# Optimization experiments

Hardware: AMD Instinct MI355X
Metric: run time of the kernel (lower is better)

The kernel has to match this reference:

```python
import jax, jax.numpy as jnp
import numpy as np
import math

B, N, IN_DIM = 128, 100, 8
E, H, FF, L = 512, 8, 2048, 6
DH = E // H
MAX_STEPS = int(N * 1.5)
EPS = 1e-5

def _ln(x, g, b):
    mu = x.mean(-1, keepdims=True)
    var = ((x - mu) ** 2).mean(-1, keepdims=True)
    return (x - mu) / jnp.sqrt(var + EPS) * g + b

def _mha(q_in, k_in, v_in, wq, bq, wk, bk, wv, bv, wo, bo):
    Bq, Sq = q_in.shape[0], q_in.shape[1]
    q = (q_in @ wq + bq).reshape(Bq, Sq, H, DH)
    k = (k_in @ wk + bk).reshape(Bq, -1, H, DH)
    v = (v_in @ wv + bv).reshape(Bq, -1, H, DH)
    s = jnp.einsum('bqhd,bkhd->bhqk', q, k) / math.sqrt(DH)
    a = jax.nn.softmax(s, axis=-1)
    o = jnp.einsum('bhqk,bkhd->bqhd', a, v).reshape(Bq, Sq, E)
    return o @ wo + bo

def setup_inputs():
    key = jax.random.key(0)
    keys = iter(jax.random.split(key, 64))
    def nrm(shape, s=0.02):
        return jax.random.normal(next(keys), shape, jnp.float32) * s
    d = {}
    d['node_features'] = jax.random.normal(next(keys), (B, N, IN_DIM), jnp.float32)
    d['edge_weights'] = jax.random.uniform(next(keys), (B, N, N), jnp.float32)
    pos = np.arange(N)[:, None].astype(np.float32)
    div = np.exp(np.arange(0, E, 2).astype(np.float32) * (-math.log(10000.0) / E))
    pe = np.zeros((N, E), np.float32)
    pe[:, 0::2] = np.sin(pos * div); pe[:, 1::2] = np.cos(pos * div)
    d['pe'] = jnp.asarray(pe)
    d['in_w'] = nrm((IN_DIM, E)); d['in_b'] = jnp.zeros((E,), jnp.float32)
    for nm in ['enc_wq', 'enc_wk', 'enc_wv', 'enc_wo']:
        d[nm] = nrm((L, E, E))
    for nm in ['enc_bq', 'enc_bk', 'enc_bv', 'enc_bo']:
        d[nm] = jnp.zeros((L, E), jnp.float32)
    d['enc_w1'] = nrm((L, E, FF)); d['enc_b1'] = jnp.zeros((L, FF), jnp.float32)
    d['enc_w2'] = nrm((L, FF, E)); d['enc_b2'] = jnp.zeros((L, E), jnp.float32)
    d['enc_ln1g'] = jnp.ones((L, E), jnp.float32); d['enc_ln1b'] = jnp.zeros((L, E), jnp.float32)
    d['enc_ln2g'] = jnp.ones((L, E), jnp.float32); d['enc_ln2b'] = jnp.zeros((L, E), jnp.float32)
    d['lstm_wih'] = nrm((E, 4 * E)); d['lstm_whh'] = nrm((E, 4 * E))
    d['lstm_bih'] = jnp.zeros((4 * E,), jnp.float32); d['lstm_bhh'] = jnp.zeros((4 * E,), jnp.float32)
    for nm in ['dec_wq', 'dec_wk', 'dec_wv', 'dec_wo', 'dec_pw']:
        d[nm] = nrm((E, E))
    for nm in ['dec_bq', 'dec_bk', 'dec_bv', 'dec_bo', 'dec_pb']:
        d[nm] = jnp.zeros((E,), jnp.float32)
    d['dec_lng'] = jnp.ones((E,), jnp.float32); d['dec_lnb'] = jnp.zeros((E,), jnp.float32)
    d['shortcut_bonus'] = jnp.asarray(5.0, jnp.float32)
    d['revisit_penalty'] = jnp.asarray(-0.5, jnp.float32)
    d['done_w'] = nrm((E, 1)); d['done_b'] = jnp.zeros((1,), jnp.float32)
    return d

def _forward(node_features, edge_weights, pe, in_w, in_b, enc_wq, enc_bq, enc_wk, enc_bk, enc_wv, enc_bv, enc_wo, enc_bo, enc_w1, enc_b1, enc_w2, enc_b2, enc_ln1g, enc_ln1b, enc_ln2g, enc_ln2b, lstm_wih, lstm_whh, lstm_bih, lstm_bhh, dec_wq, dec_bq, dec_wk, dec_bk, dec_wv, dec_bv, dec_wo, dec_bo, dec_pw, dec_pb, dec_lng, dec_lnb, shortcut_bonus, revisit_penalty, done_w, done_b):
    # ---- Encoder (dropout = eval-mode identity) ----
    x = node_features @ in_w + in_b + pe[:N]
    for l in range(L):
        attn = _mha(x, x, x, enc_wq[l], enc_bq[l], enc_wk[l], enc_bk[l], enc_wv[l], enc_bv[l], enc_wo[l], enc_bo[l])
        x = _ln(x + attn, enc_ln1g[l], enc_ln1b[l])
        ff = jax.nn.relu(x @ enc_w1[l] + enc_b1[l]) @ enc_w2[l] + enc_b2[l]
        x = _ln(x + ff, enc_ln2g[l], enc_ln2b[l])
    node_emb = x  # [B, N, E]

    ar = jnp.arange(N)
    ew_to_first = edge_weights[:, :, 0]  # dist(mid -> node 0), [B, N]

    def step_fn(carry, step):
        h, c, ctx, visited, ucount, complete, all_vis, first, prev = carry
        # LSTMCell, torch gate order (i, f, g, o)
        gates = ctx @ lstm_wih + lstm_bih + h @ lstm_whh + lstm_bhh
        i_g, f_g, g_g, o_g = jnp.split(gates, 4, axis=-1)
        c2 = jax.nn.sigmoid(f_g) * c + jax.nn.sigmoid(i_g) * jnp.tanh(g_g)
        h2 = jax.nn.sigmoid(o_g) * jnp.tanh(c2)
        # greedy done-predictor: stop if sigmoid(logit) > 0.5 once tour can be closed
        done_p = jax.nn.sigmoid(h2 @ done_w + done_b)[:, 0]
        eligible = (~complete) & (ucount >= N) & (step >= N)
        complete = complete | (eligible & (done_p > 0.5))
        # DecoderStep: 1-query attention over node embeddings
        a = _mha(h2[:, None, :], node_emb, node_emb, dec_wq, dec_bq, dec_wk, dec_bk, dec_wv, dec_bv, dec_wo, dec_bo)[:, 0]
        a = _ln(a, dec_lng, dec_lnb)
        logits = a @ dec_pw + dec_pb
        scores = jnp.einsum('be,bne->bn', logits, node_emb)
        # revisit penalty while tour incomplete (vectorized masked_fill_)
        scores = jnp.where((~all_vis)[:, None] & visited, revisit_penalty, scores)
        # shortcut bonus once all nodes visited (vectorized gather over edge_weights)
        ew_prev = jnp.take_along_axis(edge_weights, prev[:, None, None], axis=1)[:, 0, :]  # [B, N] row dist(prev -> *)
        direct = ew_prev[:, :1]                      # dist(prev -> 0)
        via = ew_prev + ew_to_first                  # dist(prev -> mid) + dist(mid -> 0)
        bonus = jnp.where(via < direct, shortcut_bonus * (direct - via) / direct, 0.0)
        scores = scores + jnp.where(all_vis[:, None], bonus, 0.0)
        # completed tours: force return to first node
        scores = jnp.where(complete[:, None], -1e9, scores)
        scores = jnp.where(complete[:, None] & (ar[None, :] == first[:, None]), 100.0, scores)
        probs = jax.nn.softmax(scores, axis=1)
        curr = jnp.argmax(probs, axis=1).astype(jnp.int32)  # greedy selection
        logp = jnp.log(jnp.take_along_axis(probs, curr[:, None], 1)[:, 0] + 1e-10)
        first = jnp.where(step == 0, curr, first)
        # state updates (guarded by active, as in the torch per-batch loop)
        active = ~complete
        cur_mask = ar[None, :] == curr[:, None]
        newly = active & ~jnp.take_along_axis(visited, curr[:, None], 1)[:, 0]
        ucount = ucount + newly.astype(jnp.int32)
        visited = visited | (active[:, None] & cur_mask)
        all_vis = all_vis | (ucount >= N)
        ctx2 = jnp.take_along_axis(node_emb, curr[:, None, None], axis=1)[:, 0, :]
        return (h2, c2, ctx2, visited, ucount, complete, all_vis, first, curr), (curr, logp)

    carry0 = (jnp.zeros((B, E), jnp.float32), jnp.zeros((B, E), jnp.float32), node_emb.mean(1),
              jnp.zeros((B, N), bool), jnp.zeros((B,), jnp.int32),
              jnp.zeros((B,), bool), jnp.zeros((B,), bool),
              jnp.zeros((B,), jnp.int32), jnp.zeros((B,), jnp.int32))
    carry, (tours, logps) = jax.lax.scan(step_fn, carry0, jnp.arange(MAX_STEPS))
    complete, first = carry[5], carry[7]
    # final forced step (step == max_steps in torch): incomplete tours return to first node, logp = 0
    final_node = jnp.where(complete, jnp.int32(0), first)
    tours = jnp.concatenate([tours, final_node[None]], 0)                 # [MAX_STEPS+1, B]
    logps = jnp.concatenate([logps, jnp.zeros((1, B), jnp.float32)], 0)   # [MAX_STEPS+1, B]
    return logps, tours

def reference(node_features, edge_weights, pe, in_w, in_b, enc_wq, enc_bq, enc_wk, enc_bk, enc_wv, enc_bv, enc_wo, enc_bo, enc_w1, enc_b1, enc_w2, enc_b2, enc_ln1g, enc_ln1b, enc_ln2g, enc_ln2b, lstm_wih, lstm_whh, lstm_bih, lstm_bhh, dec_wq, dec_bq, dec_wk, dec_bk, dec_wv, dec_bv, dec_wo, dec_bo, dec_pw, dec_pb, dec_lng, dec_lnb, shortcut_bonus, revisit_penalty, done_w, done_b):
    return _forward(node_features, edge_weights, pe, in_w, in_b, enc_wq, enc_bq, enc_wk, enc_bk, enc_wv, enc_bv, enc_wo, enc_bo, enc_w1, enc_b1, enc_w2, enc_b2, enc_ln1g, enc_ln1b, enc_ln2g, enc_ln2b, lstm_wih, lstm_whh, lstm_bih, lstm_bhh, dec_wq, dec_bq, dec_wk, dec_bk, dec_wv, dec_bv, dec_wo, dec_bo, dec_pw, dec_pb, dec_lng, dec_lnb, shortcut_bonus, revisit_penalty, done_w, done_b)
```

## Files before the change

kernel.cpp:

```cpp
#include <hip/hip_runtime.h>
#include <math.h>

#define Bb 128
#define Nn 100
#define Ee 512
#define Hh 8
#define DHd 64
#define FFf 2048
#define Ll 6
#define STEPS 150

typedef _Float16 h8 __attribute__((ext_vector_type(8)));
typedef _Float16 h4 __attribute__((ext_vector_type(4)));
typedef float f4 __attribute__((ext_vector_type(4)));

template<bool RELU, bool BIAS, bool OUTF32, bool SPLITK>
__global__ __launch_bounds__(256) void mgemm_k(
    const _Float16* __restrict__ Ah, const _Float16* __restrict__ Al, int lda,
    const _Float16* __restrict__ Bh, const _Float16* __restrict__ Bl, int ldb,
    float* __restrict__ C, _Float16* __restrict__ Ch, _Float16* __restrict__ Cl,
    int ldc, const float* __restrict__ bias, int K, int kc, int Mtot)
{
  __shared__ _Float16 sm[4 * 5120];
  _Float16* sAh = sm;
// ... 169 lines not shown
  for (int idx = t; idx < 6400; idx += 256) {
    int i = idx >> 6, d = idx & 63;
    qs[i * 68 + d]  = qg[(size_t)i * 512 + d];
    kT[d * 113 + i] = kg[(size_t)i * 512 + d];
  }
  __syncthreads();
  int ti = t >> 4, tj = t & 15;
  int i0 = ti * 7, j0 = tj * 7;
  float s[7][7];
#pragma unroll
  for (int r = 0; r < 7; ++r)
#pragma unroll
    for (int c = 0; c < 7; ++c) s[r][c] = 0.f;
  for (int kk = 0; kk < 64; ++kk) {
    float a[7], bb[7];
#pragma unroll
    for (int r = 0; r < 7; ++r) a[r] = qs[(i0 + r) * 68 + kk];
#pragma unroll
    for (int c = 0; c < 7; ++c) bb[c] = kT[kk * 113 + j0 + c];
#pragma unroll
    for (int r = 0; r < 7; ++r)
#pragma unroll
      for (int c = 0; c < 7; ++c) s[r][c] += a[r] * bb[c];
  }
  __syncthreads();
#pragma unroll
  for (int r = 0; r < 7; ++r)
#pragma unroll
    for (int c = 0; c < 7; ++c) {
      int i = i0 + r, j = j0 + c;
      if (i < Nn && j < Nn) p[i * 104 + j] = s[r][c] * 0.125f;
    }
  __syncthreads();
  int w = t >> 6, lane = t & 63;
  for (int i = w; i < Nn; i += 4) {
    float x0 = p[i * 104 + lane];
    float x1 = (lane < 36) ? p[i * 104 + 64 + lane] : -3.4e38f;
    float mx = fmaxf(x0, x1);
    for (int msk = 32; msk; msk >>= 1) mx = fmaxf(mx, __shfl_xor(mx, msk));
    float e0 = expf(x0 - mx);
    float e1 = (lane < 36) ? expf(x1 - mx) : 0.f;
    float ss = e0 + e1;
    for (int msk = 32; msk; msk >>= 1) ss += __shfl_xor(ss, msk);
    p[i * 104 + lane] = e0 / ss;
    if (lane < 36) p[i * 104 + 64 + lane] = e1 / ss;
  }
  __syncthreads();
  int d0 = tj * 4;
  float oa[7][4];
#pragma unroll
  for (int r = 0; r < 7; ++r)
#pragma unroll
    for (int c = 0; c < 4; ++c) oa[r][c] = 0.f;
  for (int j = 0; j < Nn; ++j) {
    float pr[7];
#pragma unroll
    for (int r = 0; r < 7; ++r) pr[r] = p[(i0 + r) * 104 + j];
    float4 vv = *(const float4*)(vg + (size_t)j * 512 + d0);
#pragma unroll
    for (int r = 0; r < 7; ++r) {
      oa[r][0] += pr[r] * vv.x; oa[r][1] += pr[r] * vv.y;
      oa[r][2] += pr[r] * vv.z; oa[r][3] += pr[r] * vv.w;
    }
  }
  size_t ob = ((size_t)b * Nn) * 512 + h * 64 + d0;
#pragma unroll
  for (int r = 0; r < 7; ++r)
    if (i0 + r < Nn) {
      h4 hv, lv;
#pragma unroll
      for (int c = 0; c < 4; ++c) {
        _Float16 hh = (_Float16)oa[r][c];
        hv[c] = hh;
        lv[c] = (_Float16)(oa[r][c] - (float)hh);
      }
      *(h4*)(oh + ob + (size_t)(i0 + r) * 512) = hv;
      *(h4*)(ol + ob + (size_t)(i0 + r) * 512) = lv;
    }
}

template<int BM, int BN, int BK, int TM, int TN>
__global__ __launch_bounds__(256) void gemm_k(
    const float* __restrict__ A, int lda,
    const float* __restrict__ B1, const float* __restrict__ B2, int splitB, int ldb,
    float* __restrict__ C, int ldc, int M, int N, int K, int kChunk)
{
  __shared__ __align__(16) float As[BK][BM + 4];
  __shared__ __align__(16) float Bs[BK][BN + 4];
  const int tid = threadIdx.x;
  const int m0 = blockIdx.y * BM;
  const int n0 = blockIdx.x * BN;
  const int k0 = blockIdx.z * kChunk;
  const int kEnd = k0 + kChunk;
  constexpr int TCOLS = BN / TN;
  const int tm = tid / TCOLS;
  const int tn = tid % TCOLS;
  float acc[TM][TN];
#pragma unroll
  for (int i = 0; i < TM; ++i)
#pragma unroll
    for (int j = 0; j < TN; ++j) acc[i][j] = 0.f;

  for (int kt = k0; kt < kEnd; kt += BK) {
    constexpr int A4 = BM * BK / 4;
    for (int c = tid; c < A4; c += 256) {
      int mm = c / (BK / 4);
      int k4 = (c % (BK / 4)) * 4;
      float4 av = *(const float4*)(A + (size_t)(m0 + mm) * lda + kt + k4);
      As[k4 + 0][mm] = av.x;
      As[k4 + 1][mm] = av.y;
      As[k4 + 2][mm] = av.z;
      As[k4 + 3][mm] = av.w;
    }
    constexpr int B4 = BK * BN / 4;
    for (int c = tid; c < B4; c += 256) {
      int kk = c / (BN / 4);
      int n4 = (c % (BN / 4)) * 4;
      int kgi = kt + kk;
      const float* Brow = (kgi < splitB) ? (B1 + (size_t)kgi * ldb)
                                         : (B2 + (size_t)(kgi - splitB) * ldb);
      *(float4*)&Bs[kk][n4] = *(const float4*)(Brow + n0 + n4);
    }
    __syncthreads();
#pragma unroll
    for (int kk = 0; kk < BK; ++kk) {
      float a[TM], b[TN];
#pragma unroll
      for (int i = 0; i < TM; ++i) a[i] = As[kk][tm * TM + i];
#pragma unroll
      for (int j = 0; j < TN; ++j) b[j] = Bs[kk][tn * TN + j];
#pragma unroll
      for (int i = 0; i < TM; ++i)
#pragma unroll
        for (int j = 0; j < TN; ++j)
          acc[i][j] += a[i] * b[j];
    }
    __syncthreads();
  }

  float* Cout = C + (size_t)blockIdx.z * (size_t)M * ldc;
#pragma unroll
  for (int i = 0; i < TM; ++i) {
    int m = m0 + tm * TM + i;
#pragma unroll
    for (int j = 0; j < TN; j += 4) {
      int n = n0 + tn * TN + j;
      float4 r;
      r.x = acc[i][j + 0]; r.y = acc[i][j + 1]; r.z = acc[i][j + 2]; r.w = acc[i][j + 3];
      *(float4*)(Cout + (size_t)m * ldc + n) = r;
    }
  }
}

__global__ __launch_bounds__(256) void init_k(
    const float* __restrict__ emb, float* __restrict__ ctxh, float* __restrict__ cbuf,
    int* visited, int* ucount, int* complete, int* allvis, int* first, int* prev,
    float* out)
{
  int b = blockIdx.x, t = threadIdx.x;
#pragma unroll
  for (int r = 0; r < 2; ++r) {
    int e = t + 256 * r;
    float s = 0.f;
    for (int i = 0; i < Nn; ++i) s += emb[((size_t)b * Nn + i) * 512 + e];
    ctxh[(size_t)b * 1024 + e] = s / 100.f;
    ctxh[(size_t)b * 1024 + 512 + e] = 0.f;
    cbuf[(size_t)b * 512 + e] = 0.f;
  }
  if (t < Nn) visited[b * Nn + t] = 0;
  if (t == 0) {
    ucount[b] = 0; complete[b] = 0; allvis[b] = 0; first[b] = 0; prev[b] = 0;
    out[150 * Bb + b] = 0.f;
  }
}

__device__ __forceinline__ float sigm(float x) { return 1.f / (1.f + expf(-x)); }

__global__ __launch_bounds__(256) void lstm_pw_k(
    const float* __restrict__ gP, const float* __restrict__ bih, const float* __restrict__ bhh,
    float* __restrict__ ctxh, float* __restrict__ cbuf,
    const float* __restrict__ done_w, const float* __restrict__ done_b,
    int* complete, const int* ucount, int step)
{
  int b = blockIdx.x, t = threadIdx.x;
  __shared__ float red[256];
  const float* g0 = gP + (size_t)b * 2048;
  const float* g1 = gP + 262144 + (size_t)b * 2048;
  float dsum = 0.f;
#pragma unroll
  for (int r = 0; r < 2; ++r) {
    int e = t + 256 * r;
    float ig = g0[e] + g1[e] + bih[e] + bhh[e];
    float fg = g0[e + 512] + g1[e + 512] + bih[e + 512] + bhh[e + 512];
    float gg = g0[e + 1024] + g1[e + 1024] + bih[e + 1024] + bhh[e + 1024];
    float og = g0[e + 1536] + g1[e + 1536] + bih[e + 1536] + bhh[e + 1536];
    float cprev = cbuf[(size_t)b * 512 + e];
    float c2 = sigm(fg) * cprev + sigm(ig) * tanhf(gg);
    float h2 = sigm(og) * tanhf(c2);
    cbuf[(size_t)b * 512 + e] = c2;
    ctxh[(size_t)b * 1024 + 512 + e] = h2;
    dsum += h2 * done_w[e];
  }
  red[t] = dsum; __syncthreads();
  for (int o = 128; o > 0; o >>= 1) { if (t < o) red[t] += red[t + o]; __syncthreads(); }
  if (t == 0) {
    float z = red[0] + done_b[0];
    if (!complete[b] && ucount[b] >= Nn && step >= Nn && z > 0.f) complete[b] = 1;
  }
}

__global__ __launch_bounds__(128) void dec_attn_k(
    const float* __restrict__ qP, const float* __restrict__ bq,
    const float* __restrict__ Kd, const float* __restrict__ Vd,
    float* __restrict__ o)
{
  int bh = blockIdx.x; int b = bh >> 3, h = bh & 7;
  int t = threadIdx.x;
  __shared__ float qh[64];
  __shared__ float p[100];
  __shared__ float red[128];
  if (t < 64) {
    float s = bq[h * 64 + t];
#pragma unroll
    for (int s8 = 0; s8 < 8; ++s8) s += qP[(size_t)s8 * 65536 + (size_t)b * 512 + h * 64 + t];
    qh[t] = s;
  }
  __syncthreads();
  float scv = -3.4e38f;
  if (t < Nn) {
    const float* kr = Kd + ((size_t)b * Nn + t) * 512 + h * 64;
    float s = 0.f;
#pragma unroll
    for (int d = 0; d < 64; ++d) s += qh[d] * kr[d];
    scv = s * 0.125f;
  }
  red[t] = scv; __syncthreads();
  for (int o2 = 64; o2 > 0; o2 >>= 1) { if (t < o2) red[t] = fmaxf(red[t], red[t + o2]); __syncthreads(); }
  float m = red[0]; __syncthreads();
  float ex = (t < Nn) ? expf(scv - m) : 0.f;
  red[t] = ex; __syncthreads();
  for (int o2 = 64; o2 > 0; o2 >>= 1) { if (t < o2) red[t] += red[t + o2]; __syncthreads(); }
  float Z = red[0];
  if (t < Nn) p[t] = ex / Z;
  __syncthreads();
  if (t < 64) {
    float acc = 0.f;
    const float* vr = Vd + (size_t)b * Nn * 512 + h * 64 + t;
    for (int j = 0; j < Nn; ++j) acc += p[j] * vr[(size_t)j * 512];
    o[(size_t)b * 512 + h * 64 + t] = acc;
  }
}

__global__ __launch_bounds__(256) void dec_ln_k(
    const float* __restrict__ woP, const float* __restrict__ bo,
    const float* __restrict__ g, const float* __restrict__ bb,
    float* __restrict__ out)
{
  int b = blockIdx.x, t = threadIdx.x;
  __shared__ float red[256];
  float v[2];
#pragma unroll
  for (int r = 0; r < 2; ++r) {
    int e = t + 256 * r;
    float s = bo[e];
#pragma unroll
    for (int s8 = 0; s8 < 8; ++s8) s += woP[(size_t)s8 * 65536 + (size_t)b * 512 + e];
    v[r] = s;
  }
  red[t] = v[0] + v[1]; __syncthreads();
  for (int o = 128; o > 0; o >>= 1) { if (t < o) red[t] += red[t + o]; __syncthreads(); }
  float mu = red[0] * (1.f / 512.f);
  __syncthreads();
  float d0 = v[0] - mu, d1 = v[1] - mu;
  red[t] = d0 * d0 + d1 * d1; __syncthreads();
  for (int o = 128; o > 0; o >>= 1) { if (t < o) red[t] += red[t + o]; __syncthreads(); }
  float inv = 1.f / sqrtf(red[0] * (1.f / 512.f) + 1e-5f);
  out[(size_t)b * 512 + t] = d0 * inv * g[t] + bb[t];
  out[(size_t)b * 512 + t + 256] = d1 * inv * g[t + 256] + bb[t + 256];
}

__global__ __launch_bounds__(256) void select_k(
    const float* __restrict__ pwP, const float* __restrict__ pb,
    const float* __restrict__ emb, const float* __restrict__ ew,
    int* visited, int* ucount, int* complete, int* allvis, int* first, int* prev,
    float* __restrict__ ctxh, float* __restrict__ out,
    const float* __restrict__ sb_p, const float* __restrict__ rp_p, int step)
{
  int b = blockIdx.x, t = threadIdx.x;
  __shared__ float logits[512];
  __shared__ float sc[128];
  __shared__ float red[256];
  __shared__ int redi[256];
#pragma unroll
  for (int r = 0; r < 2; ++r) {
    int e = t + 256 * r;
    float s = pb[e];
#pragma unroll
    for (int s8 = 0; s8 < 8; ++s8) s += pwP[(size_t)s8 * 65536 + (size_t)b * 512 + e];
    logits[e] = s;
  }
  __syncthreads();
  if (t < Nn) {
    const float* er = emb + ((size_t)b * Nn + t) * 512;
    float s = 0.f;
    for (int e = 0; e < 512; ++e) s += logits[e] * er[e];
    int av = allvis[b];
    if (!av && visited[b * Nn + t]) s = rp_p[0];
    if (av) {
      int pv = prev[b];
      float direct = ew[(size_t)b * 10000 + (size_t)pv * 100];
      float via = ew[(size_t)b * 10000 + (size_t)pv * 100 + t] + ew[(size_t)b * 10000 + (size_t)t * 100];
      if (via < direct) s += sb_p[0] * (direct - via) / direct;
    }
    if (complete[b]) s = (t == first[b]) ? 100.f : -1e9f;
    sc[t] = s;
  }
  __syncthreads();
  float vv = (t < Nn) ? sc[t] : -3.4e38f;
  int ii = (t < Nn) ? t : 0x7fffffff;
  red[t] = vv; redi[t] = ii;
  __syncthreads();
  for (int o = 128; o > 0; o >>= 1) {
    if (t < o) {
      float v2 = red[t + o]; int i2 = redi[t + o];
      if (v2 > red[t] || (v2 == red[t] && i2 < redi[t])) { red[t] = v2; redi[t] = i2; }
    }
    __syncthreads();
  }
  float m = red[0];
  int curr = redi[0];
  __syncthreads();
  float ex = (t < Nn) ? expf(sc[t] - m) : 0.f;
  red[t] = ex; __syncthreads();
  for (int o = 128; o > 0; o >>= 1) { if (t < o) red[t] += red[t + o]; __syncthreads(); }
  float Z = red[0];
  if (t == 0) {
    float pcur = expf(sc[curr] - m) / Z;
    out[step * Bb + b] = logf(pcur + 1e-10f);
    out[(151 + step) * Bb + b] = (float)curr;
    if (!complete[b]) {
      if (!visited[b * Nn + curr]) ucount[b] = ucount[b] + 1;
      visited[b * Nn + curr] = 1;
    }
    if (ucount[b] >= Nn) allvis[b] = 1;
    if (step == 0) first[b] = curr;
    prev[b] = curr;
  }
  const float* src = emb + ((size_t)b * Nn + curr) * 512;
  ctxh[(size_t)b * 1024 + t] = src[t];
  ctxh[(size_t)b * 1024 + t + 256] = src[t + 256];
}

__global__ void final_k(const int* complete, const int* first, float* out)
{
  int b = threadIdx.x;
  out[(151 + 150) * Bb + b] = complete[b] ? 0.f : (float)first[b];
}

extern "C" void kernel_launch(void* const* d_in, const int* in_sizes, int n_in,
                              void* d_out, int out_size, void* d_ws, size_t ws_size,
                              hipStream_t stream)
{
  const float* nf      = (const float*)d_in[0];
  const float* ew      = (const float*)d_in[1];
  const float* pe      = (const float*)d_in[2];
  const float* in_w    = (const float*)d_in[3];
  const float* in_b    = (const float*)d_in[4];
  const float* enc_wq  = (const float*)d_in[5];
  const float* enc_wk  = (const float*)d_in[6];
  const float* enc_wv  = (const float*)d_in[7];
  const float* enc_wo  = (const float*)d_in[8];
  const float* enc_bq  = (const float*)d_in[9];
  const float* enc_bk  = (const float*)d_in[10];
  const float* enc_bv  = (const float*)d_in[11];
  const float* enc_bo  = (const float*)d_in[12];
  const float* enc_w1  = (const float*)d_in[13];
  const float* enc_b1  = (const float*)d_in[14];
  const float* enc_w2  = (const float*)d_in[15];
  const float* enc_b2  = (const float*)d_in[16];
  const float* ln1g    = (const float*)d_in[17];
  const float* ln1b    = (const float*)d_in[18];
  const float* ln2g    = (const float*)d_in[19];
  const float* ln2b    = (const float*)d_in[20];
  const float* wih     = (const float*)d_in[21];
  const float* whh     = (const float*)d_in[22];
  const float* bih     = (const float*)d_in[23];
  const float* bhh     = (const float*)d_in[24];
  const float* dwq     = (const float*)d_in[25];
  const float* dwk     = (const float*)d_in[26];
  const float* dwv     = (const float*)d_in[27];
  const float* dwo     = (const float*)d_in[28];
  const float* dpw     = (const float*)d_in[29];
  const float* dbq     = (const float*)d_in[30];
  const float* dbk     = (const float*)d_in[31];
  const float* dbv     = (const float*)d_in[32];
  const float* dbo     = (const float*)d_in[33];
  const float* dpb     = (const float*)d_in[34];
  const float* dlng    = (const float*)d_in[35];
  const float* dlnb    = (const float*)d_in[36];
  const float* sbp     = (const float*)d_in[37];
  const float* rpp     = (const float*)d_in[38];
  const float* done_w  = (const float*)d_in[39];
  const float* done_b  = (const float*)d_in[40];
  float* out = (float*)d_out;

  const size_t SZ = 12800ull * 512;
  float* ws = (float*)d_ws;
  float* x   = ws;
  float* xq  = x + SZ;
  float* xk  = xq + SZ;
  float* xv  = xk + SZ;
  _Float16* xh = (_Float16*)(xv + SZ);
  _Float16* xl = xh + SZ;
  _Float16* oh = xl + SZ;
  _Float16* ol = oh + SZ;
  _Float16* wb = ol + SZ;
  _Float16* wqh = wb;               _Float16* wql = wqh + 262144;
  _Float16* wkh = wql + 262144;     _Float16* wkl = wkh + 262144;
  _Float16* wvh = wkl + 262144;     _Float16* wvl = wvh + 262144;
  _Float16* woh_ = wvl + 262144;    _Float16* wol_ = woh_ + 262144;
  _Float16* w1h = wol_ + 262144;    _Float16* w1l = w1h + 1048576;
  _Float16* w2h = w1l + 1048576;    _Float16* w2l = w2h + 1048576;
  float* ctxh   = (float*)(w2l + 1048576);
  float* cbuf   = ctxh + 131072;
  float* gatesP = cbuf + 65536;
  float* qP     = gatesP + 524288;
  float* woP    = qP + 524288;
  float* pwP    = woP + 524288;
  float* abuf   = pwP + 524288;
  float* dbuf   = abuf + 65536;
  int* ivis     = (int*)(dbuf + 65536);
  int* ucount   = ivis + 12800;
  int* complete = ucount + 128;
  int* allvis   = complete + 128;
  int* first    = allvis + 128;
  int* prev     = first + 128;

  input_proj_k<<<25600, 256, 0, stream>>>(nf, in_w, in_b, pe, x, xh, xl);

  for (int l = 0; l < Ll; ++l) {
    const float* wq = enc_wq + (size_t)l * 262144;
    const float* wk = enc_wk + (size_t)l * 262144;
    const float* wv = enc_wv + (size_t)l * 262144;
    const float* wo = enc_wo + (size_t)l * 262144;
    const float* bq = enc_bq + (size_t)l * 512;
    const float* bk = enc_bk + (size_t)l * 512;
    const float* bv = enc_bv + (size_t)l * 512;
    const float* bo = enc_bo + (size_t)l * 512;
    const float* w1 = enc_w1 + (size_t)l * 1048576;
    const float* b1 = enc_b1 + (size_t)l * 2048;
    const float* w2 = enc_w2 + (size_t)l * 1048576;
    const float* b2 = enc_b2 + (size_t)l * 512;

    wconv_k<<<dim3(16, 16), 256, 0, stream>>>(wq, 512, 512, wqh, wql);
    wconv_k<<<dim3(16, 16), 256, 0, stream>>>(wk, 512, 512, wkh, wkl);
    wconv_k<<<dim3(16, 16), 256, 0, stream>>>(wv, 512, 512, wvh, wvl);
    wconv_k<<<dim3(16, 16), 256, 0, stream>>>(wo, 512, 512, woh_, wol_);
    wconv_k<<<dim3(64, 16), 256, 0, stream>>>(w1, 512, 2048, w1h, w1l);
    wconv_k<<<dim3(16, 64), 256, 0, stream>>>(w2, 2048, 512, w2h, w2l);

    mgemm_k<false, true, true, false><<<dim3(4, 100), 256, 0, stream>>>(
        xh, xl, 512, wqh, wql, 512, xq, nullptr, nullptr, 512, bq, 512, 0, 0);
    mgemm_k<false, true, true, false><<<dim3(4, 100), 256, 0, stream>>>(
        xh, xl, 512, wkh, wkl, 512, xk, nullptr, nullptr, 512, bk, 512, 0, 0);
    mgemm_k<false, true, true, false><<<dim3(4, 100), 256, 0, stream>>>(
        xh, xl, 512, wvh, wvl, 512, xv, nullptr, nullptr, 512, bv, 512, 0, 0);
    enc_attn_k<<<1024, 256, 0, stream>>>(xq, xk, xv, oh, ol);
    mgemm_k<false, true, true, false><<<dim3(4, 100), 256, 0, stream>>>(
        oh, ol, 512, woh_, wol_, 512, xq, nullptr, nullptr, 512, bo, 512, 0, 0);
    ln_k<<<12800, 256, 0, stream>>>(x, xq, ln1g + l * 512, ln1b + l * 512, x, xh, xl);
    for (int c = 0; c < 4; ++c) {
      mgemm_k<true, true, false, false><<<dim3(16, 25), 256, 0, stream>>>(
          xh + (size_t)c * 3200 * 512, xl + (size_t)c * 3200 * 512, 512,
          w1h, w1l, 512, nullptr, oh, ol, 2048, b1, 512, 0, 0);
      mgemm_k<false, false, true, true><<<dim3(4, 25, 4), 256, 0, stream>>>(
          oh, ol, 2048, w2h, w2l, 2048, xv, nullptr, nullptr, 512,
          nullptr, 2048, 512, 3200);
      reduce4_k<<<6400, 256, 0, stream>>>(xv, b2, xq + (size_t)c * 3200 * 512);
    }
    ln_k<<<12800, 256, 0, stream>>>(x, xq, ln2g + l * 512, ln2b + l * 512, x, xh, xl);
  }

  wconv_k<<<dim3(16, 16), 256, 0, stream>>>(dwk, 512, 512, wqh, wql);
  wconv_k<<<dim3(16, 16), 256, 0, stream>>>(dwv, 512, 512, wkh, wkl);
  mgemm_k<false, true, true, false><<<dim3(4, 100), 256, 0, stream>>>(
      xh, xl, 512, wqh, wql, 512, xk, nullptr, nullptr, 512, dbk, 512, 0, 0);
  mgemm_k<false, true, true, false><<<dim3(4, 100), 256, 0, stream>>>(
      xh, xl, 512, wkh, wkl, 512, xv, nullptr, nullptr, 512, dbv, 512, 0, 0);
  init_k<<<128, 256, 0, stream>>>(x, ctxh, cbuf, ivis, ucount, complete, allvis, first, prev, out);

  for (int step = 0; step < STEPS; ++step) {
    gemm_k<32, 64, 16, 2, 4><<<dim3(32, 4, 2), 256, 0, stream>>>(
        ctxh, 1024, wih, whh, 512, 2048, gatesP, 2048, 128, 2048, 1024, 512);
    lstm_pw_k<<<128, 256, 0, stream>>>(gatesP, bih, bhh, ctxh, cbuf, done_w, done_b,
                                       complete, ucount, step);
    gemm_k<32, 64, 16, 2, 4><<<dim3(8, 4, 8), 256, 0, stream>>>(
        ctxh + 512, 1024, dwq, dwq, 1 << 30, 512, qP, 512, 128, 512, 512, 64);
    dec_attn_k<<<1024, 128, 0, stream>>>(qP, dbq, xk, xv, dbuf);
    gemm_k<32, 64, 16, 2, 4><<<dim3(8, 4, 8), 256, 0, stream>>>(
        dbuf, 512, dwo, dwo, 1 << 30, 512, woP, 512, 128, 512, 512, 64);
    dec_ln_k<<<128, 256, 0, stream>>>(woP, dbo, dlng, dlnb, abuf);
    gemm_k<32, 64, 16, 2, 4><<<dim3(8, 4, 8), 256, 0, stream>>>(
        abuf, 512, dpw, dpw, 1 << 30, 512, pwP, 512, 128, 512, 512, 64);
    select_k<<<128, 256, 0, stream>>>(pwP, dpb, x, ew, ivis, ucount, complete, allvis,
                                      first, prev, ctxh, out, sbp, rpp, step);
  }
  final_k<<<1, 128, 0, stream>>>(complete, first, out);
}
```

Baseline: 16.52 ms.

## Fuse LSTM pointwise into query GEMM and fold decoder LayerNorm into projection

The LSTM pointwise update now runs inside the query-projection GEMM, which recomputes h on the fly as its A tile and writes c into a double-buffered cell state. The done-head partial dot products go to a buffer that the select kernel reads to update completion. The decoder LayerNorm is folded algebraically into the pointer projection: the gamma-scaled weight and the gamma/beta correction vectors are precomputed once, and the LN and projection matvec are done inside the select kernel. This cuts three kernel launches and two global round-trips per decode step, at the cost of redundant LSTM math across N-blocks and a serial 512x512 matvec per batch row inside select.

```diff
diff --git a/kernel.cpp b/kernel.cpp
--- a/kernel.cpp
+++ b/kernel.cpp
@@ -345,6 +345,25 @@
   }
 }
 
+__global__ void gscale_k(const float* __restrict__ dpw, const float* __restrict__ g,
+                         float* __restrict__ gpw)
+{
+  int i = blockIdx.x * 256 + threadIdx.x;
+  gpw[i] = g[i >> 9] * dpw[i];
+}
+
+__global__ void uv_k(const float* __restrict__ pw, const float* __restrict__ g,
+                     const float* __restrict__ bb, float* __restrict__ uv)
+{
+  int c = blockIdx.x * 256 + threadIdx.x;
+  float su = 0.f, sw = 0.f;
+  for (int k = 0; k < 512; ++k) {
+    float p = pw[(size_t)k * 512 + c];
+    su += g[k] * p; sw += bb[k] * p;
+  }
+  uv[c] = su; uv[512 + c] = sw;
+}
+
 __global__ __launch_bounds__(256) void init_k(
     const float* __restrict__ emb, float* __restrict__ ctxh, float* __restrict__ cbuf,
     int* visited, int* ucount, int* complete, int* allvis, int* first, int* prev,
@@ -369,36 +388,137 @@
 
 __device__ __forceinline__ float sigm(float x) { return 1.f / (1.f + expf(-x)); }
 
-__global__ __launch_bounds__(256) void lstm_pw_k(
-    const float* __restrict__ gP, const float* __restrict__ bih, const float* __restrict__ bhh,
-    float* __restrict__ ctxh, float* __restrict__ cbuf,
-    const float* __restrict__ done_w, const float* __restrict__ done_b,
-    int* complete, const int* ucount, int step)
-{
-  int b = blockIdx.x, t = threadIdx.x;
-  __shared__ float red[256];
-  const float* g0 = gP + (size_t)b * 2048;
-  const float* g1 = gP + 262144 + (size_t)b * 2048;
-  float dsum = 0.f;
-#pragma unroll
-  for (int r = 0; r < 2; ++r) {
-    int e = t + 256 * r;
-    float ig = g0[e] + g1[e] + bih[e] + bhh[e];
-    float fg = g0[e + 512] + g1[e + 512] + bih[e + 512] + bhh[e + 512];
-    float gg = g0[e + 1024] + g1[e + 1024] + bih[e + 1024] + bhh[e + 1024];
-    float og = g0[e + 1536] + g1[e + 1536] + bih[e + 1536] + bhh[e + 1536];
-    float cprev = cbuf[(size_t)b * 512 + e];
-    float c2 = sigm(fg) * cprev + sigm(ig) * tanhf(gg);
-    float h2 = sigm(og) * tanhf(c2);
-    cbuf[(size_t)b * 512 + e] = c2;
-    ctxh[(size_t)b * 1024 + 512 + e] = h2;
-    dsum += h2 * done_w[e];
-  }
-  red[t] = dsum; __syncthreads();
-  for (int o = 128; o > 0; o >>= 1) { if (t < o) red[t] += red[t + o]; __syncthreads(); }
-  if (t == 0) {
-    float z = red[0] + done_b[0];
-    if (!complete[b] && ucount[b] >= Nn && step >= Nn && z > 0.f) complete[b] = 1;
+__device__ __forceinline__ float4 add44(float4 a, float4 b, float4 c, float4 d)
+{
+  float4 r;
+  r.x = a.x + b.x + c.x + d.x;
+  r.y = a.y + b.y + c.y + d.y;
+  r.z = a.z + b.z + c.z + d.z;
+  r.w = a.w + b.w + c.w + d.w;
+  return r;
+}
+
+__device__ __forceinline__ void lstm4(
+    const float* __restrict__ gP, const float* __restrict__ bih,
+    const float* __restrict__ bhh, const float* __restrict__ cin,
+    int b, int e4, float4* h2o, float4* c2o)
+{
+  const float* g0 = gP + (size_t)b * 2048 + e4;
+  const float* g1 = gP + 262144 + (size_t)b * 2048 + e4;
+  float4 ig = add44(*(const float4*)(g0),
+                    *(const float4*)(g1),
+                    *(const float4*)(bih + e4),
+                    *(const float4*)(bhh + e4));
+  float4 fg = add44(*(const float4*)(g0 + 512),
+                    *(const float4*)(g1 + 512),
+                    *(const float4*)(bih + 512 + e4),
+                    *(const float4*)(bhh + 512 + e4));
+  float4 gg = add44(*(const float4*)(g0 + 1024),
+                    *(const float4*)(g1 + 1024),
+                    *(const float4*)(bih + 1024 + e4),
+                    *(const float4*)(bhh + 1024 + e4));
+  float4 og = add44(*(const float4*)(g0 + 1536),
+                    *(const float4*)(g1 + 1536),
+                    *(const float4*)(bih + 1536 + e4),
+                    *(const float4*)(bhh + 1536 + e4));
+  float4 cp = *(const float4*)(cin + (size_t)b * 512 + e4);
+  float4 c2, h2;
+  c2.x = sigm(fg.x) * cp.x + sigm(ig.x) * tanhf(gg.x);  h2.x = sigm(og.x) * tanhf(c2.x);
+  c2.y = sigm(fg.y) * cp.y + sigm(ig.y) * tanhf(gg.y);  h2.y = sigm(og.y) * tanhf(c2.y);
+  c2.z = sigm(fg.z) * cp.z + sigm(ig.z) * tanhf(gg.z);  h2.z = sigm(og.z) * tanhf(c2.z);
+  c2.w = sigm(fg.w) * cp.w + sigm(ig.w) * tanhf(gg.w);  h2.w = sigm(og.w) * tanhf(c2.w);
+  *h2o = h2; *c2o = c2;
+}
+
+__global__ __launch_bounds__(256) void qh_gemm_k(
+    const float* __restrict__ gP, const float* __restrict__ bih,
+    const float* __restrict__ bhh, const float* __restrict__ cin,
+    float* __restrict__ cout, const float* __restrict__ done_w,
+    float* __restrict__ ctxh, const float* __restrict__ Bw,
+    float* __restrict__ C, float* __restrict__ dpart)
+{
+  __shared__ __align__(16) float As[16][36];
+  __shared__ __align__(16) float Bs[16][68];
+  __shared__ float sPre[32][8];
+  const int tid = threadIdx.x;
+  const int m0 = blockIdx.y * 32;
+  const int n0 = blockIdx.x * 64;
+  const int z  = blockIdx.z;
+  const int k0 = z * 64;
+  const int tm = tid >> 4;
+  const int tn = tid & 15;
+
+  if (blockIdx.x == 0) {
+    int bl = tid >> 3;
+    int el = (tid & 7) * 8;
+    int gb = m0 + bl;
+    float dsum = 0.f;
+#pragma unroll
+    for (int q = 0; q < 2; ++q) {
+      int e = k0 + el + q * 4;
+      float4 h2, c2;
+      lstm4(gP, bih, bhh, cin, gb, e, &h2, &c2);
+      *(float4*)(cout + (size_t)gb * 512 + e) = c2;
+      *(float4*)(ctxh + (size_t)gb * 1024 + 512 + e) = h2;
+      float4 dw = *(const float4*)(done_w + e);
+      dsum += h2.x * dw.x + h2.y * dw.y + h2.z * dw.z + h2.w * dw.w;
+    }
+    sPre[bl][tid & 7] = dsum;
+  }
+  __syncthreads();
+  if (blockIdx.x == 0 && tid < 32) {
+    float s = 0.f;
+#pragma unroll
+    for (int q = 0; q < 8; ++q) s += sPre[tid][q];
+    dpart[z * 128 + m0 + tid] = s;
+  }
+
+  float acc[2][4];
+#pragma unroll
+  for (int i = 0; i < 2; ++i)
+#pragma unroll
+    for (int j = 0; j < 4; ++j) acc[i][j] = 0.f;
+
+  for (int kt = k0; kt < k0 + 64; kt += 16) {
+    if (tid < 128) {
+      int mm = tid >> 2;
+      int k4 = (tid & 3) * 4;
+      float4 h2, c2d;
+      lstm4(gP, bih, bhh, cin, m0 + mm, kt + k4, &h2, &c2d);
+      As[k4 + 0][mm] = h2.x;
+      As[k4 + 1][mm] = h2.y;
+      As[k4 + 2][mm] = h2.z;
+      As[k4 + 3][mm] = h2.w;
+    }
+    {
+      int kk = tid >> 4;
+      int n4 = (tid & 15) * 4;
+      *(float4*)&Bs[kk][n4] = *(const float4*)(Bw + (size_t)(kt + kk) * 512 + n0 + n4);
+    }
+    __syncthreads();
+#pragma unroll
+    for (int kk = 0; kk < 16; ++kk) {
+      float a[2], b[4];
+      a[0] = As[kk][tm * 2 + 0];
+      a[1] = As[kk][tm * 2 + 1];
+#pragma unroll
+      for (int j = 0; j < 4; ++j) b[j] = Bs[kk][tn * 4 + j];
+#pragma unroll
+      for (int i = 0; i < 2; ++i)
+#pragma unroll
+        for (int j = 0; j < 4; ++j) acc[i][j] += a[i] * b[j];
+    }
+    __syncthreads();
+  }
+
+  float* Cout = C + (size_t)z * 128 * 512;
+#pragma unroll
+  for (int i = 0; i < 2; ++i) {
+    int m = m0 + tm * 2 + i;
+    int n = n0 + tn * 4;
+    float4 r;
+    r.x = acc[i][0]; r.y = acc[i][1]; r.z = acc[i][2]; r.w = acc[i][3];
+    *(float4*)(Cout + (size_t)m * 512 + n) = r;
   }
 }
 
@@ -444,59 +564,79 @@
   }
 }
 
-__global__ __launch_bounds__(256) void dec_ln_k(
-    const float* __restrict__ woP, const float* __restrict__ bo,
-    const float* __restrict__ g, const float* __restrict__ bb,
-    float* __restrict__ out)
-{
-  int b = blockIdx.x, t = threadIdx.x;
-  __shared__ float red[256];
-  float v[2];
-#pragma unroll
-  for (int r = 0; r < 2; ++r) {
-    int e = t + 256 * r;
-    float s = bo[e];
-#pragma unroll
-    for (int s8 = 0; s8 < 8; ++s8) s += woP[(size_t)s8 * 65536 + (size_t)b * 512 + e];
-    v[r] = s;
-  }
-  red[t] = v[0] + v[1]; __syncthreads();
-  for (int o = 128; o > 0; o >>= 1) { if (t < o) red[t] += red[t + o]; __syncthreads(); }
-  float mu = red[0] * (1.f / 512.f);
-  __syncthreads();
-  float d0 = v[0] - mu, d1 = v[1] - mu;
-  red[t] = d0 * d0 + d1 * d1; __syncthreads();
-  for (int o = 128; o > 0; o >>= 1) { if (t < o) red[t] += red[t + o]; __syncthreads(); }
-  float inv = 1.f / sqrtf(red[0] * (1.f / 512.f) + 1e-5f);
-  out[(size_t)b * 512 + t] = d0 * inv * g[t] + bb[t];
-  out[(size_t)b * 512 + t + 256] = d1 * inv * g[t + 256] + bb[t + 256];
-}
-
-__global__ __launch_bounds__(256) void select_k(
-    const float* __restrict__ pwP, const float* __restrict__ pb,
+__global__ __launch_bounds__(256) void select3_k(
+    const float* __restrict__ woP, const float* __restrict__ dbo,
+    const float* __restrict__ gpw, const float* __restrict__ uv,
+    const float* __restrict__ dpb,
     const float* __restrict__ emb, const float* __restrict__ ew,
+    const float* __restrict__ dpart, const float* __restrict__ done_b,
     int* visited, int* ucount, int* complete, int* allvis, int* first, int* prev,
     float* __restrict__ ctxh, float* __restrict__ out,
     const float* __restrict__ sb_p, const float* __restrict__ rp_p, int step)
 {
   int b = blockIdx.x, t = threadIdx.x;
-  __shared__ float logits[512];
+  __shared__ __align__(16) float yv[512];
+  __shared__ __align__(16) float lg[512];
   __shared__ float sc[128];
   __shared__ float red[256];
   __shared__ int redi[256];
-#pragma unroll
-  for (int r = 0; r < 2; ++r) {
-    int e = t + 256 * r;
-    float s = pb[e];
-#pragma unroll
-    for (int s8 = 0; s8 < 8; ++s8) s += pwP[(size_t)s8 * 65536 + (size_t)b * 512 + e];
-    logits[e] = s;
-  }
-  __syncthreads();
+  __shared__ int s_cm;
+  __shared__ float s_mu, s_inv;
+
+  if (t == 0) {
+    float dp = 0.f;
+#pragma unroll
+    for (int z = 0; z < 8; ++z) dp += dpart[z * 128 + b];
+    int cm = complete[b];
+    if (!cm && ucount[b] >= Nn && step >= Nn && (dp + done_b[0]) > 0.f) {
+      cm = 1; complete[b] = 1;
+    }
+    s_cm = cm;
+  }
+
+  float v0 = dbo[t], v1 = dbo[t + 256];
+#pragma unroll
+  for (int s8 = 0; s8 < 8; ++s8) {
+    v0 += woP[(size_t)s8 * 65536 + (size_t)b * 512 + t];
+    v1 += woP[(size_t)s8 * 65536 + (size_t)b * 512 + t + 256];
+  }
+  yv[t] = v0; yv[t + 256] = v1;
+  red[t] = v0 + v1; __syncthreads();
+  for (int o = 128; o > 0; o >>= 1) { if (t < o) red[t] += red[t + o]; __syncthreads(); }
+  float mu = red[0] * (1.f / 512.f);
+  __syncthreads();
+  float d0 = v0 - mu, d1 = v1 - mu;
+  red[t] = d0 * d0 + d1 * d1; __syncthreads();
+  for (int o = 128; o > 0; o >>= 1) { if (t < o) red[t] += red[t + o]; __syncthreads(); }
+  if (t == 0) {
+    s_mu = mu;
+    s_inv = 1.f / sqrtf(red[0] * (1.f / 512.f) + 1e-5f);
+  }
+  __syncthreads();
+
+  {
+    float acc0 = 0.f, acc1 = 0.f;
+#pragma unroll 8
+    for (int e = 0; e < 512; ++e) {
+      float ye = yv[e];
+      acc0 += ye * gpw[(size_t)e * 512 + t];
+      acc1 += ye * gpw[(size_t)e * 512 + t + 256];
+    }
+    float inv = s_inv, m2 = s_inv * s_mu;
+    lg[t]       = inv * acc0 - m2 * uv[t]       + uv[512 + t]       + dpb[t];
+    lg[t + 256] = inv * acc1 - m2 * uv[t + 256] + uv[512 + t + 256] + dpb[t + 256];
+  }
+  __syncthreads();
+
   if (t < Nn) {
     const float* er = emb + ((size_t)b * Nn + t) * 512;
     float s = 0.f;
-    for (int e = 0; e < 512; ++e) s += logits[e] * er[e];
+#pragma unroll 8
+    for (int e4 = 0; e4 < 128; ++e4) {
+      float4 ev = *(const float4*)(er + e4 * 4);
+      float4 lv = *(const float4*)(lg + e4 * 4);
+      s += lv.x * ev.x + lv.y * ev.y + lv.z * ev.z + lv.w * ev.w;
+    }
     int av = allvis[b];
     if (!av && visited[b * Nn + t]) s = rp_p[0];
     if (av) {
@@ -505,7 +645,7 @@
       float via = ew[(size_t)b * 10000 + (size_t)pv * 100 + t] + ew[(size_t)b * 10000 + (size_t)t * 100];
       if (via < direct) s += sb_p[0] * (direct - via) / direct;
     }
-    if (complete[b]) s = (t == first[b]) ? 100.f : -1e9f;
+    if (s_cm) s = (t == first[b]) ? 100.f : -1e9f;
     sc[t] = s;
   }
   __syncthreads();
@@ -531,7 +671,7 @@
     float pcur = expf(sc[curr] - m) / Z;
     out[step * Bb + b] = logf(pcur + 1e-10f);
     out[(151 + step) * Bb + b] = (float)curr;
-    if (!complete[b]) {
+    if (!s_cm) {
       if (!visited[b * Nn + curr]) ucount[b] = ucount[b] + 1;
       visited[b * Nn + curr] = 1;
     }
@@ -615,13 +755,15 @@
   _Float16* w1h = wol_ + 262144;    _Float16* w1l = w1h + 1048576;
   _Float16* w2h = w1l + 1048576;    _Float16* w2l = w2h + 1048576;
   float* ctxh   = (float*)(w2l + 1048576);
-  float* cbuf   = ctxh + 131072;
-  float* gatesP = cbuf + 65536;
+  float* cbufA  = ctxh + 131072;
+  float* gatesP = cbufA + 65536;
   float* qP     = gatesP + 524288;
   float* woP    = qP + 524288;
-  float* pwP    = woP + 524288;
-  float* abuf   = pwP + 524288;
-  float* dbuf   = abuf + 65536;
+  float* gpw    = woP + 524288;
+  float* uvv    = gpw + 262144;
+  float* dpart  = uvv + 1024;
+  float* cbufB  = gpw + 524288;
+  float* dbuf   = cbufB + 65536;
   int* ivis     = (int*)(dbuf + 65536);
   int* ucount   = ivis + 12800;
   int* complete = ucount + 128;
@@ -680,23 +822,24 @@
       xh, xl, 512, wqh, wql, 512, xk, nullptr, nullptr, 512, dbk, 512, 0, 0);
   mgemm_k<false, true, true, false><<<dim3(4, 100), 256, 0, stream>>>(
       xh, xl, 512, wkh, wkl, 512, xv, nullptr, nullptr, 512, dbv, 512, 0, 0);
-  init_k<<<128, 256, 0, stream>>>(x, ctxh, cbuf, ivis, ucount, complete, allvis, first, prev, out);
-
+  gscale_k<<<1024, 256, 0, stream>>>(dpw, dlng, gpw);
+  uv_k<<<2, 256, 0, stream>>>(dpw, dlng, dlnb, uvv);
+  init_k<<<128, 256, 0, stream>>>(x, ctxh, cbufA, ivis, ucount, complete, allvis, first, prev, out);
+
+  float* cin = cbufA;
+  float* cout = cbufB;
   for (int step = 0; step < STEPS; ++step) {
     gemm_k<32, 64, 16, 2, 4><<<dim3(32, 4, 2), 256, 0, stream>>>(
         ctxh, 1024, wih, whh, 512, 2048, gatesP, 2048, 128, 2048, 1024, 512);
-    lstm_pw_k<<<128, 256, 0, stream>>>(gatesP, bih, bhh, ctxh, cbuf, done_w, done_b,
-                                       complete, ucount, step);
-    gemm_k<32, 64, 16, 2, 4><<<dim3(8, 4, 8), 256, 0, stream>>>(
-        ctxh + 512, 1024, dwq, dwq, 1 << 30, 512, qP, 512, 128, 512, 512, 64);
+    qh_gemm_k<<<dim3(8, 4, 8), 256, 0, stream>>>(
+        gatesP, bih, bhh, cin, cout, done_w, ctxh, dwq, qP, dpart);
     dec_attn_k<<<1024, 128, 0, stream>>>(qP, dbq, xk, xv, dbuf);
     gemm_k<32, 64, 16, 2, 4><<<dim3(8, 4, 8), 256, 0, stream>>>(
         dbuf, 512, dwo, dwo, 1 << 30, 512, woP, 512, 128, 512, 512, 64);
-    dec_ln_k<<<128, 256, 0, stream>>>(woP, dbo, dlng, dlnb, abuf);
-    gemm_k<32, 64, 16, 2, 4><<<dim3(8, 4, 8), 256, 0, stream>>>(
-        abuf, 512, dpw, dpw, 1 << 30, 512, pwP, 512, 128, 512, 512, 64);
-    select_k<<<128, 256, 0, stream>>>(pwP, dpb, x, ew, ivis, ucount, complete, allvis,
-                                      first, prev, ctxh, out, sbp, rpp, step);
+    select3_k<<<128, 256, 0, stream>>>(woP, dbo, gpw, uvv, dpb, x, ew, dpart, done_b,
+                                       ivis, ucount, complete, allvis, first, prev,
+                                       ctxh, out, sbp, rpp, step);
+    float* tmp = cin; cin = cout; cout = tmp;
   }
   final_k<<<1, 128, 0, stream>>>(complete, first, out);
 }
```

New measurement: 20.04 ms. +21.3%, slower.

## Fuse LSTM gate GEMM with pointwise cell update using interleaved gate weights

Applied to the files above, without the earlier changes.

Builds an interleaved weight matrix so each output column group holds the i/f/g/o gates of one hidden unit. The LSTM gate GEMM and pointwise cell update then run in a single kernel per step, replacing a split-K GEMM plus a separate pointwise kernel and removing the gatesP round trip. The hidden state is double-buffered across steps to avoid a read/write race. The done-probe reduction moves into select_k via per-block partial sums. The fused kernel loses split-K parallelism (128 blocks over K=1024), which may lengthen the per-step serial chain.

```diff
diff --git a/kernel.cpp b/kernel.cpp
--- a/kernel.cpp
+++ b/kernel.cpp
@@ -345,6 +345,17 @@
   }
 }
 
+__global__ void wg2build_k(const float* __restrict__ wih, const float* __restrict__ whh,
+                           float* __restrict__ Wg2)
+{
+  int idx = blockIdx.x * 256 + threadIdx.x;
+  int k = idx >> 9, e = idx & 511;
+  const float* src = (k < 512) ? (wih + (size_t)k * 2048) : (whh + (size_t)(k - 512) * 2048);
+  float4 o;
+  o.x = src[e]; o.y = src[512 + e]; o.z = src[1024 + e]; o.w = src[1536 + e];
+  *(float4*)(Wg2 + (size_t)k * 2048 + e * 4) = o;
+}
+
 __global__ __launch_bounds__(256) void init_k(
     const float* __restrict__ emb, float* __restrict__ ctxh, float* __restrict__ cbuf,
     int* visited, int* ucount, int* complete, int* allvis, int* first, int* prev,
@@ -356,8 +367,8 @@
     int e = t + 256 * r;
     float s = 0.f;
     for (int i = 0; i < Nn; ++i) s += emb[((size_t)b * Nn + i) * 512 + e];
-    ctxh[(size_t)b * 1024 + e] = s / 100.f;
-    ctxh[(size_t)b * 1024 + 512 + e] = 0.f;
+    ctxh[(size_t)b * 1536 + e] = s / 100.f;
+    ctxh[(size_t)b * 1536 + 512 + e] = 0.f;
     cbuf[(size_t)b * 512 + e] = 0.f;
   }
   if (t < Nn) visited[b * Nn + t] = 0;
@@ -369,36 +380,85 @@
 
 __device__ __forceinline__ float sigm(float x) { return 1.f / (1.f + expf(-x)); }
 
-__global__ __launch_bounds__(256) void lstm_pw_k(
-    const float* __restrict__ gP, const float* __restrict__ bih, const float* __restrict__ bhh,
-    float* __restrict__ ctxh, float* __restrict__ cbuf,
-    const float* __restrict__ done_w, const float* __restrict__ done_b,
-    int* complete, const int* ucount, int step)
-{
-  int b = blockIdx.x, t = threadIdx.x;
-  __shared__ float red[256];
-  const float* g0 = gP + (size_t)b * 2048;
-  const float* g1 = gP + 262144 + (size_t)b * 2048;
-  float dsum = 0.f;
-#pragma unroll
-  for (int r = 0; r < 2; ++r) {
-    int e = t + 256 * r;
-    float ig = g0[e] + g1[e] + bih[e] + bhh[e];
-    float fg = g0[e + 512] + g1[e + 512] + bih[e + 512] + bhh[e + 512];
-    float gg = g0[e + 1024] + g1[e + 1024] + bih[e + 1024] + bhh[e + 1024];
-    float og = g0[e + 1536] + g1[e + 1536] + bih[e + 1536] + bhh[e + 1536];
-    float cprev = cbuf[(size_t)b * 512 + e];
-    float c2 = sigm(fg) * cprev + sigm(ig) * tanhf(gg);
+__global__ __launch_bounds__(256) void gateslstm_k(
+    const float* __restrict__ ctxh_c, const float* __restrict__ Wg2,
+    const float* __restrict__ bih, const float* __restrict__ bhh,
+    float* __restrict__ cbuf, const float* __restrict__ done_w,
+    float* __restrict__ ctxh_w, float* __restrict__ dpart, int hin)
+{
+  __shared__ __align__(16) float As[16][36];
+  __shared__ __align__(16) float Bs[16][68];
+  __shared__ float sDD[32][17];
+  const int tid = threadIdx.x;
+  const int m0 = blockIdx.y * 32;
+  const int n0 = blockIdx.x * 64;
+  const int tm = tid >> 4;
+  const int tn = tid & 15;
+  float acc[2][4];
+#pragma unroll
+  for (int i = 0; i < 2; ++i)
+#pragma unroll
+    for (int j = 0; j < 4; ++j) acc[i][j] = 0.f;
+
+  for (int kt = 0; kt < 1024; kt += 16) {
+    const int akt = kt + ((kt >= 512) ? 512 * hin : 0);
+    if (tid < 128) {
+      int mm = tid >> 2;
+      int k4 = (tid & 3) * 4;
+      float4 av = *(const float4*)(ctxh_c + (size_t)(m0 + mm) * 1536 + akt + k4);
+      As[k4 + 0][mm] = av.x;
+      As[k4 + 1][mm] = av.y;
+      As[k4 + 2][mm] = av.z;
+      As[k4 + 3][mm] = av.w;
+    }
+    {
+      int kk = tid >> 4;
+      int n4 = (tid & 15) * 4;
+      *(float4*)&Bs[kk][n4] = *(const float4*)(Wg2 + (size_t)(kt + kk) * 2048 + n0 + n4);
+    }
+    __syncthreads();
+#pragma unroll
+    for (int kk = 0; kk < 16; ++kk) {
+      float a[2], b[4];
+      a[0] = As[kk][tm * 2 + 0];
+      a[1] = As[kk][tm * 2 + 1];
+#pragma unroll
+      for (int j = 0; j < 4; ++j) b[j] = Bs[kk][tn * 4 + j];
+#pragma unroll
+      for (int i = 0; i < 2; ++i)
+#pragma unroll
+        for (int j = 0; j < 4; ++j) acc[i][j] += a[i] * b[j];
+    }
+    __syncthreads();
+  }
+
+  const int e = (n0 >> 2) + tn;
+  const float bi0 = bih[e],        bh0 = bhh[e];
+  const float bi1 = bih[512 + e],  bh1 = bhh[512 + e];
+  const float bi2 = bih[1024 + e], bh2 = bhh[1024 + e];
+  const float bi3 = bih[1536 + e], bh3 = bhh[1536 + e];
+  const float dw = done_w[e];
+  const int hwoff = 512 + 512 * (hin ^ 1);
+#pragma unroll
+  for (int i = 0; i < 2; ++i) {
+    int b = m0 + tm * 2 + i;
+    float ig = acc[i][0] + bi0 + bh0;
+    float fg = acc[i][1] + bi1 + bh1;
+    float gg = acc[i][2] + bi2 + bh2;
+    float og = acc[i][3] + bi3 + bh3;
+    float cp = cbuf[(size_t)b * 512 + e];
+    float c2 = sigm(fg) * cp + sigm(ig) * tanhf(gg);
     float h2 = sigm(og) * tanhf(c2);
     cbuf[(size_t)b * 512 + e] = c2;
-    ctxh[(size_t)b * 1024 + 512 + e] = h2;
-    dsum += h2 * done_w[e];
-  }
-  red[t] = dsum; __syncthreads();
-  for (int o = 128; o > 0; o >>= 1) { if (t < o) red[t] += red[t + o]; __syncthreads(); }
-  if (t == 0) {
-    float z = red[0] + done_b[0];
-    if (!complete[b] && ucount[b] >= Nn && step >= Nn && z > 0.f) complete[b] = 1;
+    ctxh_w[(size_t)b * 1536 + hwoff + e] = h2;
+    sDD[tm * 2 + i][tn] = h2 * dw;
+  }
+  __syncthreads();
+  if (tid < 32) {
+    float s = 0.f;
+#pragma unroll
+    for (int q = 0; q < 16; ++q) s += sDD[tid][q];
+    dpart[(size_t)blockIdx.x * 128 + m0 + tid] = s;
   }
 }
 
@@ -475,6 +535,7 @@
 __global__ __launch_bounds__(256) void select_k(
     const float* __restrict__ pwP, const float* __restrict__ pb,
     const float* __restrict__ emb, const float* __restrict__ ew,
+    const float* __restrict__ dpart, const float* __restrict__ done_b,
     int* visited, int* ucount, int* complete, int* allvis, int* first, int* prev,
     float* __restrict__ ctxh, float* __restrict__ out,
     const float* __restrict__ sb_p, const float* __restrict__ rp_p, int step)
@@ -484,6 +545,17 @@
   __shared__ float sc[128];
   __shared__ float red[256];
   __shared__ int redi[256];
+  __shared__ int s_cm;
+  if (t == 0) {
+    float dp = 0.f;
+#pragma unroll
+    for (int j2 = 0; j2 < 32; ++j2) dp += dpart[(size_t)j2 * 128 + b];
+    int cm = complete[b];
+    if (!cm && ucount[b] >= Nn && step >= Nn && (dp + done_b[0]) > 0.f) {
+      cm = 1; complete[b] = 1;
+    }
+    s_cm = cm;
+  }
 #pragma unroll
   for (int r = 0; r < 2; ++r) {
     int e = t + 256 * r;
@@ -505,7 +577,7 @@
       float via = ew[(size_t)b * 10000 + (size_t)pv * 100 + t] + ew[(size_t)b * 10000 + (size_t)t * 100];
       if (via < direct) s += sb_p[0] * (direct - via) / direct;
     }
-    if (complete[b]) s = (t == first[b]) ? 100.f : -1e9f;
+    if (s_cm) s = (t == first[b]) ? 100.f : -1e9f;
     sc[t] = s;
   }
   __syncthreads();
@@ -531,7 +603,7 @@
     float pcur = expf(sc[curr] - m) / Z;
     out[step * Bb + b] = logf(pcur + 1e-10f);
     out[(151 + step) * Bb + b] = (float)curr;
-    if (!complete[b]) {
+    if (!s_cm) {
       if (!visited[b * Nn + curr]) ucount[b] = ucount[b] + 1;
       visited[b * Nn + curr] = 1;
     }
@@ -540,8 +612,8 @@
     prev[b] = curr;
   }
   const float* src = emb + ((size_t)b * Nn + curr) * 512;
-  ctxh[(size_t)b * 1024 + t] = src[t];
-  ctxh[(size_t)b * 1024 + t + 256] = src[t + 256];
+  ctxh[(size_t)b * 1536 + t] = src[t];
+  ctxh[(size_t)b * 1536 + t + 256] = src[t + 256];
 }
 
 __global__ void final_k(const int* complete, const int* first, float* out)
@@ -615,9 +687,9 @@
   _Float16* w1h = wol_ + 262144;    _Float16* w1l = w1h + 1048576;
   _Float16* w2h = w1l + 1048576;    _Float16* w2l = w2h + 1048576;
   float* ctxh   = (float*)(w2l + 1048576);
-  float* cbuf   = ctxh + 131072;
-  float* gatesP = cbuf + 65536;
-  float* qP     = gatesP + 524288;
+  float* cbuf   = ctxh + 196608;
+  float* dpart  = cbuf + 65536;
+  float* qP     = dpart + 4096;
   float* woP    = qP + 524288;
   float* pwP    = woP + 524288;
   float* abuf   = pwP + 524288;
@@ -680,22 +752,25 @@
       xh, xl, 512, wqh, wql, 512, xk, nullptr, nullptr, 512, dbk, 512, 0, 0);
   mgemm_k<false, true, true, false><<<dim3(4, 100), 256, 0, stream>>>(
       xh, xl, 512, wkh, wkl, 512, xv, nullptr, nullptr, 512, dbv, 512, 0, 0);
+
+  float* Wg2 = (float*)wb;
+  wg2build_k<<<2048, 256, 0, stream>>>(wih, whh, Wg2);
   init_k<<<128, 256, 0, stream>>>(x, ctxh, cbuf, ivis, ucount, complete, allvis, first, prev, out);
 
   for (int step = 0; step < STEPS; ++step) {
-    gemm_k<32, 64, 16, 2, 4><<<dim3(32, 4, 2), 256, 0, stream>>>(
-        ctxh, 1024, wih, whh, 512, 2048, gatesP, 2048, 128, 2048, 1024, 512);
-    lstm_pw_k<<<128, 256, 0, stream>>>(gatesP, bih, bhh, ctxh, cbuf, done_w, done_b,
-                                       complete, ucount, step);
+    int hin = step & 1;
+    gateslstm_k<<<dim3(32, 4), 256, 0, stream>>>(
+        ctxh, Wg2, bih, bhh, cbuf, done_w, ctxh, dpart, hin);
     gemm_k<32, 64, 16, 2, 4><<<dim3(8, 4, 8), 256, 0, stream>>>(
-        ctxh + 512, 1024, dwq, dwq, 1 << 30, 512, qP, 512, 128, 512, 512, 64);
+        ctxh + 512 + 512 * (hin ^ 1), 1536, dwq, dwq, 1 << 30, 512, qP, 512, 128, 512, 512, 64);
     dec_attn_k<<<1024, 128, 0, stream>>>(qP, dbq, xk, xv, dbuf);
     gemm_k<32, 64, 16, 2, 4><<<dim3(8, 4, 8), 256, 0, stream>>>(
         dbuf, 512, dwo, dwo, 1 << 30, 512, woP, 512, 128, 512, 512, 64);
     dec_ln_k<<<128, 256, 0, stream>>>(woP, dbo, dlng, dlnb, abuf);
     gemm_k<32, 64, 16, 2, 4><<<dim3(8, 4, 8), 256, 0, stream>>>(
         abuf, 512, dpw, dpw, 1 << 30, 512, pwP, 512, 128, 512, 512, 64);
-    select_k<<<128, 256, 0, stream>>>(pwP, dpb, x, ew, ivis, ucount, complete, allvis,
+    select_k<<<128, 256, 0, stream>>>(pwP, dpb, x, ew, dpart, done_b,
+                                      ivis, ucount, complete, allvis,
                                       first, prev, ctxh, out, sbp, rpp, step);
   }
   final_k<<<1, 128, 0, stream>>>(complete, first, out);
```

New measurement: 21.54 ms. 30.3% more time.
